# Optimization experiments

Measured on AMD Instinct MI355X. Metric: run time of the kernel, lower is better.

The kernel has to match this reference:

```python
import jax, jax.numpy as jnp
import numpy as np

DIM = 128
HEADS = 4
KV_RANK = 64
Q_RANK = 32
ROPE = DIM // 2   # 64
NOPE = DIM // 2   # 64
VDIM = DIM // 2   # 64
B, H, W = 2, 64, 64
EPS = 1e-5


def _conv1x1(x, w, b):
    # x: [B,C,H,W], w: [O,C], b: [O]
    return jnp.einsum('bchw,oc->bohw', x, w) + b[None, :, None, None]


def _gn1(x, g, b):
    # GroupNorm with 1 group: normalize over (C,H,W) per sample
    mu = jnp.mean(x, axis=(1, 2, 3), keepdims=True)
    var = jnp.mean((x - mu) ** 2, axis=(1, 2, 3), keepdims=True)
    return (x - mu) / jnp.sqrt(var + EPS) * g[None, :, None, None] + b[None, :, None, None]


def _freqs(h, w):
    # Replicates RotaryPositionalEncoding: pe[...,0::4]=sin_h, 1::4=cos_h, 2::4=sin_w, 3::4=cos_w
    n = ROPE // 4
    inv = 1.0 / (10000.0 ** (jnp.arange(n, dtype=jnp.float32) / n))
    ah = jnp.arange(h, dtype=jnp.float32)[:, None] * inv  # [h,n]
    aw = jnp.arange(w, dtype=jnp.float32)[:, None] * inv  # [w,n]
    fh = jnp.stack([jnp.sin(ah), jnp.cos(ah)], -1)  # [h,n,2] -> (real=sin_h, imag=cos_h)
    fw = jnp.stack([jnp.sin(aw), jnp.cos(aw)], -1)  # [w,n,2]
    fh_b = jnp.broadcast_to(fh[:, None], (h, w, n, 2))
    fw_b = jnp.broadcast_to(fw[None, :], (h, w, n, 2))
    # interleave pairs: pair 2m -> fh[m], pair 2m+1 -> fw[m]
    pe = jnp.stack([fh_b, fw_b], axis=3).reshape(h * w, ROPE // 2, 2)
    return pe  # [S, ROPE//2, 2]


def _rope(x, f):
    # x: [..., S, ROPE]; f: [S, ROPE//2, 2]
    xp = x.reshape(x.shape[:-1] + (ROPE // 2, 2))
    fr, fi = f[..., 0], f[..., 1]  # [S, ROPE//2] broadcast over leading dims
    rr = xp[..., 0] * fr - xp[..., 1] * fi
    ri = xp[..., 0] * fi + xp[..., 1] * fr
    return jnp.stack([rr, ri], -1).reshape(x.shape)


def setup_inputs() -> dict:
    key = jax.random.key(0)
    ks = jax.random.split(key, 8)
    s = 0.02
    inp = {
        'x': jax.random.normal(ks[0], (B, DIM, H, W), dtype=jnp.float32),
        'q1_w': jax.random.normal(ks[1], (Q_RANK, DIM), dtype=jnp.float32) * s,
        'q1_b': jnp.zeros((Q_RANK,), jnp.float32),
        'q_gn_g': jnp.ones((Q_RANK,), jnp.float32),
        'q_gn_b': jnp.zeros((Q_RANK,), jnp.float32),
        'q2_w': jax.random.normal(ks[2], (HEADS * (NOPE + ROPE), Q_RANK), dtype=jnp.float32) * s,
        'q2_b': jnp.zeros((HEADS * (NOPE + ROPE),), jnp.float32),
        'kv1_w': jax.random.normal(ks[3], (KV_RANK + ROPE, DIM), dtype=jnp.float32) * s,
        'kv1_b': jnp.zeros((KV_RANK + ROPE,), jnp.float32),
        'kv_gn_g': jnp.ones((KV_RANK + ROPE,), jnp.float32),
        'kv_gn_b': jnp.zeros((KV_RANK + ROPE,), jnp.float32),
        'kvn_g': jnp.ones((KV_RANK,), jnp.float32),
        'kvn_b': jnp.zeros((KV_RANK,), jnp.float32),
        'kvup_w': jax.random.normal(ks[4], (HEADS * (NOPE + VDIM), KV_RANK), dtype=jnp.float32) * s,
        'kvup_b': jnp.zeros((HEADS * (NOPE + VDIM),), jnp.float32),
        'out_w': jax.random.normal(ks[5], (DIM, HEADS * VDIM), dtype=jnp.float32) * s,
        'out_b': jnp.zeros((DIM,), jnp.float32),
    }
    return inp


def reference(x, q1_w, q1_b, q_gn_g, q_gn_b, q2_w, q2_b, kv1_w, kv1_b, kv_gn_g, kv_gn_b, kvn_g, kvn_b, kvup_w, kvup_b, out_w, out_b):
    b, c, h, w = x.shape
    s = h * w
    f = _freqs(h, w)  # [S, ROPE//2, 2]

    # Q path: low-rank down -> GN -> up
    q = _conv1x1(_gn1(_conv1x1(x, q1_w, q1_b), q_gn_g, q_gn_b), q2_w, q2_b)
    q = q.reshape(b, HEADS, NOPE + ROPE, s).transpose(0, 1, 3, 2)  # [B,H,S,D]
    q_nope, q_rope = q[..., :NOPE], q[..., NOPE:]
    q = jnp.concatenate([q_nope, _rope(q_rope, f)], axis=-1)

    # KV path: joint down-proj, split rope-k and compressed kv
    kv = _gn1(_conv1x1(x, kv1_w, kv1_b), kv_gn_g, kv_gn_b)  # [B, ROPE+KV_RANK, H, W]
    k_rope_c, kv_c = kv[:, :ROPE], kv[:, ROPE:]
    kv_u = _conv1x1(_gn1(kv_c, kvn_g, kvn_b), kvup_w, kvup_b)
    kv_u = kv_u.reshape(b, HEADS, NOPE + VDIM, s).transpose(0, 1, 3, 2)
    k_nope, v = kv_u[..., :NOPE], kv_u[..., NOPE:]

    k_rope = _rope(k_rope_c.reshape(b, ROPE, s).transpose(0, 2, 1)[:, None], f)  # [B,1,S,ROPE]
    k = jnp.concatenate([k_nope, jnp.broadcast_to(k_rope, (b, HEADS, s, ROPE))], axis=-1)

    scale = (NOPE + ROPE) ** -0.5
    attn = jax.nn.softmax(jnp.einsum('bhqd,bhkd->bhqk', q, k) * scale, axis=-1)
    o = jnp.einsum('bhqk,bhkd->bhqd', attn, v)  # [B,H,S,VDIM]
    o = o.transpose(0, 1, 3, 2).reshape(b, HEADS * VDIM, h, w)
    return _conv1x1(o, out_w, out_b) + x
```

## Files before the change

kernel.cpp:

```cpp
#include <hip/hip_runtime.h>

typedef unsigned short ushort_t;
typedef unsigned int uint_t;
typedef __attribute__((ext_vector_type(8))) short s16x8;
typedef __attribute__((ext_vector_type(4))) short s16x4;
typedef __attribute__((ext_vector_type(4))) float f32x4;
typedef __attribute__((ext_vector_type(16))) float f32x16;

#define S_TOT 4096
#define QSCALE 0.08838834764831845f
#define LOG2E 1.4426950408889634f
#define QSL (QSCALE * LOG2E)
#define L2_10000_D16 0.8304820237218406f

__device__ __forceinline__ ushort_t f2b(float f) {
  uint_t u = __float_as_uint(f);
  uint_t r = (u + 0x7FFFu + ((u >> 16) & 1u)) >> 16;
  return (ushort_t)r;
}

__device__ __forceinline__ float b2f(ushort_t u) {
  return __uint_as_float((uint_t)u << 16);
}

__device__ __forceinline__ uint_t cvt_pk_bf16(float lo, float hi) {
  uint_t r;
  asm("v_cvt_pk_bf16_f32 %0, %1, %2" : "=v"(r) : "v"(lo), "v"(hi));
  return r;
}

__device__ __forceinline__ void gload16(const void* g, void* l) {
  __builtin_amdgcn_global_load_lds(
      (const __attribute__((address_space(1))) unsigned int*)g,
      (__attribute__((address_space(3))) unsigned int*)l, 16, 0, 0);
}

__device__ __forceinline__ void rope_pair(float& x0, float& x1, int p, int hi, int wi, float scale) {
  float inv = exp2f(-(float)(p >> 1) * L2_10000_D16);
  float ang = ((p & 1) ? (float)wi : (float)hi) * inv;
  float sn = sinf(ang), cs = cosf(ang);
  float r0 = (x0 * sn - x1 * cs) * scale;
  float r1 = (x0 * cs + x1 * sn) * scale;
  x0 = r0; x1 = r1;
}

__global__ __launch_bounds__(256) void k_conv1(
    const float* __restrict__ x, const float* __restrict__ q1_w, const float* __restrict__ q1_b,
    const float* __restrict__ kv1_w, const float* __restrict__ kv1_b,
    float* __restrict__ y_q, float* __restrict__ y_kv, double* __restrict__ pch,
    const float* __restrict__ q2_w, const float* __restrict__ kvup_w,
    const float* __restrict__ out_w, ushort_t* __restrict__ wq2,
    ushort_t* __restrict__ wkvup, ushort_t* __restrict__ wout) {
  if (blockIdx.x >= 512) {
    int i = (blockIdx.x - 512) * 256 + threadIdx.x;
    if (i < 16384) wq2[i] = f2b(q2_w[i]);
    else if (i < 49152) wkvup[i - 16384] = f2b(kvup_w[i - 16384]);
    else if (i < 81920) wout[i - 49152] = f2b(out_w[i - 49152]);
    return;
  }
  const int b = blockIdx.x >> 8, blk = blockIdx.x & 255, st = blk * 16;
  const int t = threadIdx.x, si = t & 15, g = t >> 4;
  __shared__ float xs[128][16];
#pragma unroll
  for (int i = 0; i < 8; i++) {
    int c = g + 16 * i;
    xs[c][si] = x[(size_t)(b * 128 + c) * S_TOT + st + si];
  }
  __syncthreads();
  float acc[10];
#pragma unroll
  for (int i = 0; i < 10; i++) {
    int oc = g * 10 + i;
    acc[i] = (oc < 32) ? q1_b[oc] : kv1_b[oc - 32];
  }
  const float4* q1w4 = (const float4*)q1_w;
  const float4* kv1w4 = (const float4*)kv1_w;
  for (int c4 = 0; c4 < 32; c4++) {
    float x0 = xs[c4 * 4 + 0][si], x1 = xs[c4 * 4 + 1][si];
    float x2 = xs[c4 * 4 + 2][si], x3 = xs[c4 * 4 + 3][si];
#pragma unroll
    for (int i = 0; i < 10; i++) {
      int oc = g * 10 + i;
      float4 wv = (oc < 32) ? q1w4[oc * 32 + c4] : kv1w4[(oc - 32) * 32 + c4];
      acc[i] += wv.x * x0 + wv.y * x1 + wv.z * x2 + wv.w * x3;
    }
  }
#pragma unroll
  for (int i = 0; i < 10; i++) {
    int oc = g * 10 + i;
    float a = acc[i];
    if (oc < 32) y_q[(size_t)(b * 32 + oc) * S_TOT + st + si] = a;
    else         y_kv[(size_t)(b * 128 + oc - 32) * S_TOT + st + si] = a;
    double s = a, q = (double)a * a;
#pragma unroll
    for (int o = 1; o < 16; o <<= 1) { s += __shfl_xor(s, o, 16); q += __shfl_xor(q, o, 16); }
    if (si == 0) {
      double* pt = pch + (size_t)(b * 160 + oc) * 512 + blk * 2;
      pt[0] = s; pt[1] = q;
    }
  }
}

__global__ __launch_bounds__(256) void k_red(
    const double* __restrict__ pch, double* __restrict__ SQ) {
  const int pair = blockIdx.x, tid = threadIdx.x;
  const int lane = tid & 63, wid = tid >> 6;
  const double* p = pch + (size_t)pair * 512;
  double s = p[tid * 2], q = p[tid * 2 + 1];
#pragma unroll
  for (int o = 1; o < 64; o <<= 1) { s += __shfl_xor(s, o, 64); q += __shfl_xor(q, o, 64); }
  __shared__ double red[4][2];
  if (lane == 0) { red[wid][0] = s; red[wid][1] = q; }
  __syncthreads();
  if (tid == 0) {
    SQ[pair * 2]     = red[0][0] + red[1][0] + red[2][0] + red[3][0];
    SQ[pair * 2 + 1] = red[0][1] + red[1][1] + red[2][1] + red[3][1];
  }
}

__global__ __launch_bounds__(512) void k_stats(
    const double* __restrict__ SQ,
    const float* __restrict__ qg, const float* __restrict__ qb,
    const float* __restrict__ kvg, const float* __restrict__ kvb,
    const float* __restrict__ kng, const float* __restrict__ knb,
    float* __restrict__ coef) {
  __shared__ double Sh[2][160], Qh[2][160];
  const int tid = threadIdx.x;
  if (tid < 320) {
    int b = tid / 160, c = tid % 160;
    Sh[b][c] = SQ[tid * 2]; Qh[b][c] = SQ[tid * 2 + 1];
  }
  __syncthreads();
  if (tid < 2) {
    int b = tid;
    float* cf = coef + b * 320;
    const double NS = 4096.0;
    double muq = 0, m2q = 0;
    for (int c = 0; c < 32; c++) { muq += Sh[b][c]; m2q += Qh[b][c]; }
    muq /= (32.0 * NS); m2q /= (32.0 * NS);
    double rstdq = 1.0 / sqrt(m2q - muq * muq + 1e-5);
    for (int c = 0; c < 32; c++) {
      double A = rstdq * (double)qg[c];
      cf[c] = (float)A; cf[32 + c] = (float)((double)qb[c] - muq * A);
    }
    double mukv = 0, m2kv = 0;
    for (int c = 0; c < 128; c++) { mukv += Sh[b][32 + c]; m2kv += Qh[b][32 + c]; }
    mukv /= (128.0 * NS); m2kv /= (128.0 * NS);
    double rstdkv = 1.0 / sqrt(m2kv - mukv * mukv + 1e-5);
    for (int c = 0; c < 64; c++) {
      double A = rstdkv * (double)kvg[c];
      cf[64 + c] = (float)A; cf[128 + c] = (float)((double)kvb[c] - mukv * A);
    }
    double mu2 = 0, m22 = 0;
    for (int c2 = 0; c2 < 64; c2++) {
      int c = 64 + c2;
      double a = rstdkv * (double)kvg[c], bb = (double)kvb[c] - mukv * a;
      double Ec = Sh[b][32 + c] / NS, M2c = Qh[b][32 + c] / NS;
      mu2 += a * Ec + bb;
      m22 += a * a * M2c + 2.0 * a * bb * Ec + bb * bb;
    }
    mu2 /= 64.0; m22 /= 64.0;
    double rstd2 = 1.0 / sqrt(m22 - mu2 * mu2 + 1e-5);
    for (int c2 = 0; c2 < 64; c2++) {
      int c = 64 + c2;
      double a = rstdkv * (double)kvg[c], bb = (double)kvb[c] - mukv * a;
      cf[192 + c2] = (float)(a * rstd2 * (double)kng[c2]);
      cf[256 + c2] = (float)((bb - mu2) * rstd2 * (double)kng[c2] + (double)knb[c2]);
    }
  }
}

__global__ __launch_bounds__(256) void k_gq(
    const float* __restrict__ y_q, const float* __restrict__ coef,
    const ushort_t* __restrict__ wq2, const float* __restrict__ q2_b,
    ushort_t* __restrict__ Q) {
  const int id = blockIdx.x;
  const int h = id & 3, st = (id >> 2) & 63, b = id >> 8;
  const int t = threadIdx.x, si = t & 63, wid = t >> 6;
  const int l15 = t & 15, lg = (t >> 4) & 3;
  const float* cf = coef + b * 320;
  __shared__ __align__(16) ushort_t Xt[64][64];
  __shared__ __align__(16) ushort_t sQ[64][128];
  {
    ushort_t pk[8];
#pragma unroll
    for (int j = 0; j < 8; j++) {
      int c = wid * 8 + j;
      float v = y_q[(size_t)(b * 32 + c) * S_TOT + st * 64 + si];
      pk[j] = f2b(v * cf[c] + cf[32 + c]);
    }
    *(s16x8*)((char*)&Xt[si][0] + ((wid * 16) ^ ((si & 7) << 4))) = *(s16x8*)pk;
  }
  __syncthreads();
  const int d0w = wid * 32;
  f32x4 acc[2][4];
#pragma unroll
  for (int db = 0; db < 2; db++) {
    f32x4 bv;
#pragma unroll
    for (int r = 0; r < 4; r++) bv[r] = q2_b[h * 128 + d0w + db * 16 + lg * 4 + r];
#pragma unroll
    for (int sb = 0; sb < 4; sb++) acc[db][sb] = bv;
  }
  s16x8 wf[2];
#pragma unroll
  for (int db = 0; db < 2; db++)
    wf[db] = *(const s16x8*)(wq2 + (size_t)(h * 128 + d0w + db * 16 + l15) * 32 + lg * 8);
  const int xsw = (lg * 16) ^ ((l15 & 7) << 4);
#pragma unroll
  for (int sb = 0; sb < 4; sb++) {
    s16x8 xf = *(const s16x8*)((const char*)&Xt[sb * 16 + l15][0] + xsw);
#pragma unroll
    for (int db = 0; db < 2; db++)
      acc[db][sb] = __builtin_amdgcn_mfma_f32_16x16x32_bf16(wf[db], xf, acc[db][sb], 0, 0, 0);
  }
  if (wid >= 2) {
#pragma unroll
    for (int db = 0; db < 2; db++)
#pragma unroll
      for (int sb = 0; sb < 4; sb++) {
        int sp = st * 64 + sb * 16 + l15, hi = sp >> 6, wi = sp & 63;
        int dg = d0w + db * 16 + lg * 4;
#pragma unroll
        for (int pr = 0; pr < 2; pr++) {
          float v0 = acc[db][sb][pr * 2], v1 = acc[db][sb][pr * 2 + 1];
          int p = (dg + pr * 2 - 64) >> 1;
          rope_pair(v0, v1, p, hi, wi, QSL);
          acc[db][sb][pr * 2] = v0; acc[db][sb][pr * 2 + 1] = v1;
        }
      }
  } else {
#pragma unroll
    for (int db = 0; db < 2; db++)
#pragma unroll
      for (int sb = 0; sb < 4; sb++)
#pragma unroll
        for (int r = 0; r < 4; r++) acc[db][sb][r] *= QSL;
  }
#pragma unroll
  for (int db = 0; db < 2; db++)
#pragma unroll
    for (int sb = 0; sb < 4; sb++) {
      ushort_t pk[4];
#pragma unroll
      for (int r = 0; r < 4; r++) pk[r] = f2b(acc[db][sb][r]);
      int srow = sb * 16 + l15;
      *(s16x4*)((char*)&sQ[srow][0] + (((d0w + db * 16 + lg * 4) * 2) ^ ((srow & 7) << 4))) =
          *(s16x4*)pk;
    }
  __syncthreads();
  ushort_t* qrow = Q + ((size_t)(b * 4 + h) * S_TOT + st * 64 + si) * 128 + wid * 32;
#pragma unroll
  for (int j = 0; j < 4; j++) {
    s16x8 v = *(const s16x8*)((const char*)&sQ[si][0] + ((wid * 64 + j * 16) ^ ((si & 7) << 4)));
    *(s16x8*)(qrow + j * 8) = v;
  }
}

__global__ __launch_bounds__(256) void k_gkv(
    const float* __restrict__ y_kv, const float* __restrict__ coef,
    const ushort_t* __restrict__ wkvup, const float* __restrict__ kvup_b,
    ushort_t* __restrict__ K, ushort_t* __restrict__ VT) {
  const int id = blockIdx.x;
  const int h = id & 3, st = (id >> 2) & 63, b = id >> 8;
  const int t = threadIdx.x, si = t & 63, wid = t >> 6;
  const int l15 = t & 15, lg = (t >> 4) & 3;
  const float* cf = coef + b * 320;
  __shared__ __align__(16) ushort_t Xt[64][64];
  __shared__ __align__(16) ushort_t sK[64][64];
  {
#pragma unroll
    for (int half = 0; half < 2; half++) {
      ushort_t pk[8];
#pragma unroll
      for (int j = 0; j < 8; j++) {
        int c2 = wid * 16 + half * 8 + j;
        float v = y_kv[(size_t)(b * 128 + 64 + c2) * S_TOT + st * 64 + si];
        pk[j] = f2b(v * cf[192 + c2] + cf[256 + c2]);
      }
      *(s16x8*)((char*)&Xt[si][0] + ((wid * 32 + half * 16) ^ ((si & 7) << 4))) = *(s16x8*)pk;
    }
  }
  __syncthreads();
  const int d0w = wid * 32;
  f32x4 acc[2][4];
#pragma unroll
  for (int db = 0; db < 2; db++) {
    f32x4 bv;
#pragma unroll
    for (int r = 0; r < 4; r++) bv[r] = kvup_b[h * 128 + d0w + db * 16 + lg * 4 + r];
#pragma unroll
    for (int sb = 0; sb < 4; sb++) acc[db][sb] = bv;
  }
  s16x8 wf[2][2];
#pragma unroll
  for (int db = 0; db < 2; db++)
#pragma unroll
    for (int kk = 0; kk < 2; kk++)
      wf[db][kk] = *(const s16x8*)(wkvup + (size_t)(h * 128 + d0w + db * 16 + l15) * 64 +
                                   kk * 32 + lg * 8);
#pragma unroll
  for (int sb = 0; sb < 4; sb++) {
#pragma unroll
    for (int kk = 0; kk < 2; kk++) {
      s16x8 xf = *(const s16x8*)((const char*)&Xt[sb * 16 + l15][0] +
                                 ((kk * 64 + lg * 16) ^ ((l15 & 7) << 4)));
#pragma unroll
      for (int db = 0; db < 2; db++)
        acc[db][sb] = __builtin_amdgcn_mfma_f32_16x16x32_bf16(wf[db][kk], xf, acc[db][sb], 0, 0, 0);
    }
  }
  if (wid < 2) {
#pragma unroll
    for (int db = 0; db < 2; db++)
#pragma unroll
      for (int sb = 0; sb < 4; sb++) {
        ushort_t pk[4];
#pragma unroll
        for (int r = 0; r < 4; r++) pk[r] = f2b(acc[db][sb][r]);
        int srow = sb * 16 + l15;
        *(s16x4*)((char*)&sK[srow][0] + (((d0w + db * 16 + lg * 4) * 2) ^ ((srow & 7) << 4))) =
            *(s16x4*)pk;
      }
  } else {
    ushort_t* vb = VT + (size_t)(b * 4 + h) * 64 * S_TOT;
#pragma unroll
    for (int db = 0; db < 2; db++)
#pragma unroll
      for (int sb = 0; sb < 4; sb++) {
        int sp = st * 64 + sb * 16 + l15;
#pragma unroll
        for (int r = 0; r < 4; r++) {
          int vd = (wid - 2) * 32 + db * 16 + lg * 4 + r;
          vb[(size_t)vd * S_TOT + sp] = f2b(acc[db][sb][r]);
        }
      }
  }
  __syncthreads();
  const int sp = st * 64 + si;
  ushort_t* krow = K + ((size_t)(b * 4 + h) * S_TOT + sp) * 128;
#pragma unroll
  for (int j = 0; j < 2; j++) {
    s16x8 v = *(const s16x8*)((const char*)&sK[si][0] + ((wid * 32 + j * 16) ^ ((si & 7) << 4)));
    *(s16x8*)(krow + wid * 16 + j * 8) = v;
  }
  {
    const int c0 = wid * 16, hi = sp >> 6, wi = sp & 63;
    float v[16];
#pragma unroll
    for (int j = 0; j < 16; j++) {
      int c = c0 + j;
      v[j] = y_kv[(size_t)(b * 128 + c) * S_TOT + sp] * cf[64 + c] + cf[128 + c];
    }
#pragma unroll
    for (int k = 0; k < 8; k++) {
      int p = (c0 >> 1) + k;
      rope_pair(v[2 * k], v[2 * k + 1], p, hi, wi, 1.0f);
    }
    ushort_t pk[16];
#pragma unroll
    for (int j = 0; j < 16; j++) pk[j] = f2b(v[j]);
    *(s16x8*)(krow + 64 + c0) = *(s16x8*)pk;
    *(s16x8*)(krow + 64 + c0 + 8) = *(s16x8*)(pk + 8);
  }
}

__global__ __launch_bounds__(256, 2) void k_attn(
    const ushort_t* __restrict__ Q, const ushort_t* __restrict__ K,
    const ushort_t* __restrict__ VT, ushort_t* __restrict__ Opart,
    float* __restrict__ ml) {
  const int bid = blockIdx.x;
  const int bh = bid & 7;
  const int rest = bid >> 3;
  const int half = rest >> 5, qblk = rest & 31;
  const int kv0 = half * 2048;
  const int tid = threadIdx.x;
  const int wid = tid >> 6, lane = tid & 63;
  const int l31 = lane & 31, hi = lane >> 5;
  const int qbase = qblk * 128 + wid * 32;
  const ushort_t* Qp = Q + (size_t)bh * S_TOT * 128;
  const ushort_t* Kp = K + (size_t)bh * S_TOT * 128;
  const ushort_t* Vp = VT + (size_t)bh * 64 * S_TOT;

  __shared__ __align__(16) ushort_t K_lds[3][64][128];
  __shared__ __align__(16) ushort_t V_lds[3][64][64];

  s16x8 qf[8];
#pragma unroll
  for (int c = 0; c < 8; c++)
    qf[c] = *(const s16x8*)(Qp + (size_t)(qbase + l31) * 128 + c * 16 + hi * 8);

  f32x16 o0, o1;
#pragma unroll
  for (int r = 0; r < 16; r++) { o0[r] = 0.f; o1[r] = 0.f; }
  float m_s = -1e30f, l_s = 0.f;

  const int krow_l = tid >> 4;
  const int kcolb = (tid & 15) * 16;
  const int vrow_l = tid >> 3;
  const int vcolb = (tid & 7) * 16;

#define STAGE(kvb, bufi)                                                          \
  {                                                                               \
    _Pragma("unroll")                                                             \
    for (int i = 0; i < 4; i++) {                                                 \
      int row = i * 16 + krow_l;                                                  \
      int colb = kcolb ^ ((row & 15) << 4);                                       \
      gload16((const char*)(Kp + (size_t)((kvb) + row) * 128) + colb,             \
              (void*)&K_lds[bufi][i * 16 + wid * 4][0]);                          \
    }                                                                             \
    _Pragma("unroll")                                                             \
    for (int i = 0; i < 2; i++) {                                                 \
      int vd = i * 32 + vrow_l;                                                   \
      int colb = vcolb ^ ((vd & 7) << 4);                                         \
      gload16((const char*)(Vp + (size_t)vd * S_TOT + (kvb)) + colb,              \
              (void*)&V_lds[bufi][i * 32 + wid * 8][0]);                          \
    }                                                                             \
  }

  STAGE(kv0, 0);
  STAGE(kv0 + 64, 1);

  const int kswz = (l31 & 15) << 4;
  const int vswz = (l31 & 7) << 4;
#pragma unroll 1
  for (int t = 0; t < 32; t++) {
    const int buf = t % 3;
    if (t < 31) {
      asm volatile("s_waitcnt vmcnt(6)" ::: "memory");
    } else {
      asm volatile("s_waitcnt vmcnt(0)" ::: "memory");
    }
    __builtin_amdgcn_sched_barrier(0);
    __builtin_amdgcn_s_barrier();
    __builtin_amdgcn_sched_barrier(0);
    if (t < 30) STAGE(kv0 + (t + 2) * 64, (t + 2) % 3);
    f32x16 sc0, sc1;
#pragma unroll
    for (int r = 0; r < 16; r++) { sc0[r] = 0.f; sc1[r] = 0.f; }
    __builtin_amdgcn_s_setprio(1);
#pragma unroll
    for (int c = 0; c < 8; c++) {
      const int off = (c * 32 + hi * 16) ^ kswz;
      s16x8 k0 = *(const s16x8*)((const char*)&K_lds[buf][l31][0] + off);
      s16x8 k1 = *(const s16x8*)((const char*)&K_lds[buf][32 + l31][0] + off);
      sc0 = __builtin_amdgcn_mfma_f32_32x32x16_bf16(k0, qf[c], sc0, 0, 0, 0);
      sc1 = __builtin_amdgcn_mfma_f32_32x32x16_bf16(k1, qf[c], sc1, 0, 0, 0);
    }
    __builtin_amdgcn_s_setprio(0);
    float pmax;
    {
      float a = fmaxf(sc0[0], sc0[1]);
#pragma unroll
      for (int r = 2; r < 16; r++) a = fmaxf(a, sc0[r]);
#pragma unroll
      for (int r = 0; r < 16; r++) a = fmaxf(a, sc1[r]);
      pmax = a;
    }
    pmax = fmaxf(pmax, __shfl_xor(pmax, 32, 64));
    if (__any(pmax - m_s > 11.5f)) {
      float mn = fmaxf(m_s, pmax);
      float alpha = exp2f(m_s - mn);
      m_s = mn;
      l_s *= alpha;
#pragma unroll
      for (int r = 0; r < 16; r++) { o0[r] *= alpha; o1[r] *= alpha; }
    }
    float rs = 0.f;
#pragma unroll
    for (int r = 0; r < 16; r++) {
      float p0 = exp2f(sc0[r] - m_s);
      float p1 = exp2f(sc1[r] - m_s);
      sc0[r] = p0; sc1[r] = p1;
      rs += p0 + p1;
    }
    l_s += rs;
    __builtin_amdgcn_s_setprio(1);
#pragma unroll
    for (int c = 0; c < 4; c++) {
      const f32x16 P = (c < 2) ? sc0 : sc1;
      const int rA = 8 * (c & 1);
      uint_t a0 = cvt_pk_bf16(P[rA + 0], P[rA + 1]);
      uint_t a1 = cvt_pk_bf16(P[rA + 2], P[rA + 3]);
      uint_t b0 = cvt_pk_bf16(P[rA + 4], P[rA + 5]);
      uint_t b1 = cvt_pk_bf16(P[rA + 6], P[rA + 7]);
      uint_t s0 = hi ? a0 : b0, s1 = hi ? a1 : b1;
      uint_t r0 = (uint_t)__shfl_xor((int)s0, 32, 64);
      uint_t r1 = (uint_t)__shfl_xor((int)s1, 32, 64);
      union { uint_t u[4]; s16x8 v; } pf;
      pf.u[0] = hi ? r0 : a0; pf.u[1] = hi ? r1 : a1;
      pf.u[2] = hi ? b0 : r0; pf.u[3] = hi ? b1 : r1;
      const int voff = (c * 32 + hi * 16) ^ vswz;
      s16x8 v0 = *(const s16x8*)((const char*)&V_lds[buf][l31][0] + voff);
      s16x8 v1 = *(const s16x8*)((const char*)&V_lds[buf][32 + l31][0] + voff);
      o0 = __builtin_amdgcn_mfma_f32_32x32x16_bf16(v0, pf.v, o0, 0, 0, 0);
      o1 = __builtin_amdgcn_mfma_f32_32x32x16_bf16(v1, pf.v, o1, 0, 0, 0);
    }
    __builtin_amdgcn_s_setprio(0);
  }
#undef STAGE
  l_s += __shfl_xor(l_s, 32, 64);
  float linv = 1.f / l_s;
  if (lane < 32) {
    float* mlrow = ml + ((size_t)(half * 8 + bh) * S_TOT + qbase + l31) * 2;
    mlrow[0] = m_s; mlrow[1] = l_s;
  }
  char* sO = (char*)&K_lds[0][0][0];
#pragma unroll
  for (int vt = 0; vt < 2; vt++) {
#pragma unroll
    for (int r = 0; r < 16; r += 2) {
      float v0 = (vt ? o1[r] : o0[r]) * linv;
      float v1 = (vt ? o1[r + 1] : o0[r + 1]) * linv;
      uint_t u = cvt_pk_bf16(v0, v1);
      int vd = vt * 32 + (r & 3) + 8 * (r >> 2) + 4 * hi;
      *(uint_t*)(sO + (wid * 32 + l31) * 128 + ((vd * 2) ^ ((l31 & 7) << 4))) = u;
    }
  }
  __syncthreads();
  {
    const int r = tid >> 1, hf = tid & 1;
    const int w = r >> 5, ql = r & 31;
    ushort_t* orow = Opart + ((size_t)(half * 8 + bh) * S_TOT + qblk * 128 + r) * 64 + hf * 32;
#pragma unroll
    for (int j = 0; j < 4; j++) {
      s16x8 v = *(const s16x8*)(sO + (w * 32 + ql) * 128 + ((hf * 64 + j * 16) ^ ((ql & 7) << 4)));
      *(s16x8*)(orow + j * 8) = v;
    }
  }
}

__global__ __launch_bounds__(256) void k_oc(
    const ushort_t* __restrict__ Opart, const float* __restrict__ ml,
    const ushort_t* __restrict__ wout, const float* __restrict__ out_b,
    const float* __restrict__ x, float* __restrict__ out) {
  const int id = blockIdx.x;
  const int cch = id & 1, st32 = (id >> 1) & 127, b = id >> 8;
  const int t = threadIdx.x, wid = t >> 6;
  const int l15 = t & 15, lg = (t >> 4) & 3;
  __shared__ __align__(16) ushort_t Xt[32][256];
  {
    const int s = t & 31, grp = t >> 5;
    const int h = grp >> 1, vd0 = (grp & 1) * 32;
    const int sp = st32 * 32 + s;
    const float2 ml0 = *(const float2*)&ml[((size_t)(b * 4 + h) * S_TOT + sp) * 2];
    const float2 ml1 = *(const float2*)&ml[((size_t)(8 + b * 4 + h) * S_TOT + sp) * 2];
    float mm = fmaxf(ml0.x, ml1.x);
    float w0 = exp2f(ml0.x - mm) * ml0.y, w1 = exp2f(ml1.x - mm) * ml1.y;
    float inv = 1.f / (w0 + w1);
    w0 *= inv; w1 *= inv;
    const ushort_t* oa = Opart + ((size_t)(b * 4 + h) * S_TOT + sp) * 64 + vd0;
    const ushort_t* obp = oa + (size_t)8 * S_TOT * 64;
#pragma unroll
    for (int j4 = 0; j4 < 4; j4++) {
      union { s16x8 v; ushort_t u[8]; } av, bv2;
      av.v = *(const s16x8*)(oa + j4 * 8);
      bv2.v = *(const s16x8*)(obp + j4 * 8);
      ushort_t pk[8];
#pragma unroll
      for (int j = 0; j < 8; j++) pk[j] = f2b(w0 * b2f(av.u[j]) + w1 * b2f(bv2.u[j]));
      *(s16x8*)((char*)&Xt[s][0] + ((grp * 64 + j4 * 16) ^ ((s & 7) << 4))) = *(s16x8*)pk;
    }
  }
  __syncthreads();
  const int c0w = cch * 64 + wid * 16;
  f32x4 acc[2];
  {
    f32x4 bv;
#pragma unroll
    for (int r = 0; r < 4; r++) bv[r] = out_b[c0w + lg * 4 + r];
    acc[0] = bv; acc[1] = bv;
  }
#pragma unroll
  for (int kk = 0; kk < 8; kk++) {
    s16x8 wf = *(const s16x8*)(wout + (size_t)(c0w + l15) * 256 + kk * 32 + lg * 8);
#pragma unroll
    for (int sb = 0; sb < 2; sb++) {
      s16x8 xf = *(const s16x8*)((const char*)&Xt[sb * 16 + l15][0] +
                                 ((kk * 64 + lg * 16) ^ ((l15 & 7) << 4)));
      acc[sb] = __builtin_amdgcn_mfma_f32_16x16x32_bf16(wf, xf, acc[sb], 0, 0, 0);
    }
  }
#pragma unroll
  for (int sb = 0; sb < 2; sb++) {
#pragma unroll
    for (int r = 0; r < 4; r++) {
      int c = c0w + lg * 4 + r;
      int sp = st32 * 32 + sb * 16 + l15;
      size_t idx = (size_t)(b * 128 + c) * S_TOT + sp;
      out[idx] = acc[sb][r] + x[idx];
    }
  }
}

extern "C" void kernel_launch(void* const* d_in, const int* in_sizes, int n_in,
                              void* d_out, int out_size, void* d_ws, size_t ws_size,
                              hipStream_t stream) {
  const float* x      = (const float*)d_in[0];
  const float* q1_w   = (const float*)d_in[1];
  const float* q1_b   = (const float*)d_in[2];
  const float* q_gn_g = (const float*)d_in[3];
  const float* q_gn_b = (const float*)d_in[4];
  const float* q2_w   = (const float*)d_in[5];
  const float* q2_b   = (const float*)d_in[6];
  const float* kv1_w  = (const float*)d_in[7];
  const float* kv1_b  = (const float*)d_in[8];
  const float* kv_gn_g= (const float*)d_in[9];
  const float* kv_gn_b= (const float*)d_in[10];
  const float* kvn_g  = (const float*)d_in[11];
  const float* kvn_b  = (const float*)d_in[12];
  const float* kvup_w = (const float*)d_in[13];
  const float* kvup_b = (const float*)d_in[14];
  const float* out_w  = (const float*)d_in[15];
  const float* out_b  = (const float*)d_in[16];

  const size_t MB = 1u << 20;
  char* ws = (char*)d_ws;
  float*    y_q   = (float*)(ws);
  float*    y_kv  = (float*)(ws + 1 * MB);
  ushort_t* Q     = (ushort_t*)(ws + 5 * MB);
  ushort_t* K     = (ushort_t*)(ws + 13 * MB);
  ushort_t* VT    = (ushort_t*)(ws + 21 * MB);
  double*   pch   = (double*)(ws + 25 * MB);
  double*   SQ    = (double*)(ws + 26 * MB + 524288);
  float*    coef  = (float*)(ws + 26 * MB + 532480);
  ushort_t* wq2   = (ushort_t*)(ws + 26 * MB + 540672);
  ushort_t* wkvup = (ushort_t*)(ws + 26 * MB + 573440);
  ushort_t* wout  = (ushort_t*)(ws + 26 * MB + 638976);
  ushort_t* Opart = (ushort_t*)(ws + 27 * MB);
  float*    ml    = (float*)(ws + 36 * MB);
  float*    out   = (float*)d_out;

  k_conv1<<<832, 256, 0, stream>>>(x, q1_w, q1_b, kv1_w, kv1_b, y_q, y_kv, pch,
                                   q2_w, kvup_w, out_w, wq2, wkvup, wout);
  k_red  <<<320, 256, 0, stream>>>(pch, SQ);
  k_stats<<<1,   512, 0, stream>>>(SQ, q_gn_g, q_gn_b, kv_gn_g, kv_gn_b, kvn_g, kvn_b, coef);
  k_gq   <<<512, 256, 0, stream>>>(y_q, coef, wq2, q2_b, Q);
  k_gkv  <<<512, 256, 0, stream>>>(y_kv, coef, wkvup, kvup_b, K, VT);
  k_attn <<<512, 256, 0, stream>>>(Q, K, VT, Opart, ml);
  k_oc   <<<512, 256, 0, stream>>>(Opart, ml, wout, out_b, x, out);
}
```

Measured before the change: 152.4 us.

## Absorb kv up-projection into Q and output weights, share latent KV across heads

Folds the kv up-projection weights into the q2 projection (nope part) and the output projection, so attention operates directly on a shared per-batch latent KV instead of per-head K and V. The per-head K/V generation GEMM kernel is replaced by a light latent-normalization kernel, cutting K/V memory footprint and traffic by the head count. Weight folding is done on-device in the first kernel's spare blocks; the K-side bias is dropped as softmax-invariant and the V bias folded into the output bias. Risks slight numeric differences from bf16 rounding of folded weights and a low-parallelism latent kernel with strided writes.

```diff
diff --git a/kernel.cpp b/kernel.cpp
--- a/kernel.cpp
+++ b/kernel.cpp
@@ -48,14 +48,52 @@
     const float* __restrict__ x, const float* __restrict__ q1_w, const float* __restrict__ q1_b,
     const float* __restrict__ kv1_w, const float* __restrict__ kv1_b,
     float* __restrict__ y_q, float* __restrict__ y_kv, double* __restrict__ pch,
-    const float* __restrict__ q2_w, const float* __restrict__ kvup_w,
-    const float* __restrict__ out_w, ushort_t* __restrict__ wq2,
-    ushort_t* __restrict__ wkvup, ushort_t* __restrict__ wout) {
+    const float* __restrict__ q2_w, const float* __restrict__ q2_b,
+    const float* __restrict__ kvup_w, const float* __restrict__ kvup_b,
+    const float* __restrict__ out_w, const float* __restrict__ out_b,
+    ushort_t* __restrict__ wq2, ushort_t* __restrict__ wout,
+    float* __restrict__ q2b2, float* __restrict__ outb2) {
   if (blockIdx.x >= 512) {
-    int i = (blockIdx.x - 512) * 256 + threadIdx.x;
-    if (i < 16384) wq2[i] = f2b(q2_w[i]);
-    else if (i < 49152) wkvup[i - 16384] = f2b(kvup_w[i - 16384]);
-    else if (i < 81920) wout[i - 49152] = f2b(out_w[i - 49152]);
+    int E = (blockIdx.x - 512) * 256 + threadIdx.x;
+    if (E < 16384) {
+      int oc = E >> 5, r = E & 31;
+      int h = oc >> 7, d = oc & 127;
+      float val;
+      if (d < 64) {
+        val = 0.f;
+        for (int dd = 0; dd < 64; dd++)
+          val += kvup_w[(h * 128 + dd) * 64 + d] * q2_w[(size_t)(h * 128 + dd) * 32 + r];
+      } else {
+        val = q2_w[(size_t)oc * 32 + r];
+      }
+      wq2[(size_t)oc * 32 + r] = f2b(val);
+    } else if (E < 49152) {
+      int e = E - 16384;
+      int c = e >> 8, col = e & 255;
+      int h = col >> 6, l = col & 63;
+      float val = 0.f;
+      for (int vd = 0; vd < 64; vd++)
+        val += out_w[(size_t)c * 256 + h * 64 + vd] * kvup_w[(h * 128 + 64 + vd) * 64 + l];
+      wout[(size_t)c * 256 + col] = f2b(val);
+    } else if (E < 49664) {
+      int oc = E - 49152;
+      int h = oc >> 7, d = oc & 127;
+      float val;
+      if (d < 64) {
+        val = 0.f;
+        for (int dd = 0; dd < 64; dd++)
+          val += kvup_w[(h * 128 + dd) * 64 + d] * q2_b[h * 128 + dd];
+      } else val = q2_b[oc];
+      q2b2[oc] = val;
+    } else if (E < 49792) {
+      int c = E - 49664;
+      float val = out_b[c];
+      for (int j = 0; j < 256; j++) {
+        int h = j >> 6, vd = j & 63;
+        val += out_w[(size_t)c * 256 + j] * kvup_b[h * 128 + 64 + vd];
+      }
+      outb2[c] = val;
+    }
     return;
   }
   const int b = blockIdx.x >> 8, blk = blockIdx.x & 255, st = blk * 16;
@@ -172,7 +210,7 @@
 
 __global__ __launch_bounds__(256) void k_gq(
     const float* __restrict__ y_q, const float* __restrict__ coef,
-    const ushort_t* __restrict__ wq2, const float* __restrict__ q2_b,
+    const ushort_t* __restrict__ wq2, const float* __restrict__ q2b2,
     ushort_t* __restrict__ Q) {
   const int id = blockIdx.x;
   const int h = id & 3, st = (id >> 2) & 63, b = id >> 8;
@@ -198,7 +236,7 @@
   for (int db = 0; db < 2; db++) {
     f32x4 bv;
 #pragma unroll
-    for (int r = 0; r < 4; r++) bv[r] = q2_b[h * 128 + d0w + db * 16 + lg * 4 + r];
+    for (int r = 0; r < 4; r++) bv[r] = q2b2[h * 128 + d0w + db * 16 + lg * 4 + r];
 #pragma unroll
     for (int sb = 0; sb < 4; sb++) acc[db][sb] = bv;
   }
@@ -257,116 +295,51 @@
   }
 }
 
-__global__ __launch_bounds__(256) void k_gkv(
+__global__ __launch_bounds__(256) void k_lat(
     const float* __restrict__ y_kv, const float* __restrict__ coef,
-    const ushort_t* __restrict__ wkvup, const float* __restrict__ kvup_b,
-    ushort_t* __restrict__ K, ushort_t* __restrict__ VT) {
-  const int id = blockIdx.x;
-  const int h = id & 3, st = (id >> 2) & 63, b = id >> 8;
-  const int t = threadIdx.x, si = t & 63, wid = t >> 6;
-  const int l15 = t & 15, lg = (t >> 4) & 3;
+    ushort_t* __restrict__ C, ushort_t* __restrict__ VT) {
+  const int blk = blockIdx.x;
+  const int b = blk >> 6, st = (blk & 63) * 64;
+  const int t = threadIdx.x, si = t & 63, g = t >> 6;
   const float* cf = coef + b * 320;
-  __shared__ __align__(16) ushort_t Xt[64][64];
-  __shared__ __align__(16) ushort_t sK[64][64];
-  {
-#pragma unroll
-    for (int half = 0; half < 2; half++) {
-      ushort_t pk[8];
-#pragma unroll
-      for (int j = 0; j < 8; j++) {
-        int c2 = wid * 16 + half * 8 + j;
-        float v = y_kv[(size_t)(b * 128 + 64 + c2) * S_TOT + st * 64 + si];
-        pk[j] = f2b(v * cf[192 + c2] + cf[256 + c2]);
-      }
-      *(s16x8*)((char*)&Xt[si][0] + ((wid * 32 + half * 16) ^ ((si & 7) << 4))) = *(s16x8*)pk;
-    }
-  }
-  __syncthreads();
-  const int d0w = wid * 32;
-  f32x4 acc[2][4];
-#pragma unroll
-  for (int db = 0; db < 2; db++) {
-    f32x4 bv;
-#pragma unroll
-    for (int r = 0; r < 4; r++) bv[r] = kvup_b[h * 128 + d0w + db * 16 + lg * 4 + r];
-#pragma unroll
-    for (int sb = 0; sb < 4; sb++) acc[db][sb] = bv;
-  }
-  s16x8 wf[2][2];
-#pragma unroll
-  for (int db = 0; db < 2; db++)
-#pragma unroll
-    for (int kk = 0; kk < 2; kk++)
-      wf[db][kk] = *(const s16x8*)(wkvup + (size_t)(h * 128 + d0w + db * 16 + l15) * 64 +
-                                   kk * 32 + lg * 8);
-#pragma unroll
-  for (int sb = 0; sb < 4; sb++) {
-#pragma unroll
-    for (int kk = 0; kk < 2; kk++) {
-      s16x8 xf = *(const s16x8*)((const char*)&Xt[sb * 16 + l15][0] +
-                                 ((kk * 64 + lg * 16) ^ ((l15 & 7) << 4)));
-#pragma unroll
-      for (int db = 0; db < 2; db++)
-        acc[db][sb] = __builtin_amdgcn_mfma_f32_16x16x32_bf16(wf[db][kk], xf, acc[db][sb], 0, 0, 0);
-    }
-  }
-  if (wid < 2) {
-#pragma unroll
-    for (int db = 0; db < 2; db++)
-#pragma unroll
-      for (int sb = 0; sb < 4; sb++) {
-        ushort_t pk[4];
-#pragma unroll
-        for (int r = 0; r < 4; r++) pk[r] = f2b(acc[db][sb][r]);
-        int srow = sb * 16 + l15;
-        *(s16x4*)((char*)&sK[srow][0] + (((d0w + db * 16 + lg * 4) * 2) ^ ((srow & 7) << 4))) =
-            *(s16x4*)pk;
-      }
-  } else {
-    ushort_t* vb = VT + (size_t)(b * 4 + h) * 64 * S_TOT;
-#pragma unroll
-    for (int db = 0; db < 2; db++)
-#pragma unroll
-      for (int sb = 0; sb < 4; sb++) {
-        int sp = st * 64 + sb * 16 + l15;
-#pragma unroll
-        for (int r = 0; r < 4; r++) {
-          int vd = (wid - 2) * 32 + db * 16 + lg * 4 + r;
-          vb[(size_t)vd * S_TOT + sp] = f2b(acc[db][sb][r]);
-        }
-      }
-  }
-  __syncthreads();
-  const int sp = st * 64 + si;
-  ushort_t* krow = K + ((size_t)(b * 4 + h) * S_TOT + sp) * 128;
-#pragma unroll
-  for (int j = 0; j < 2; j++) {
-    s16x8 v = *(const s16x8*)((const char*)&sK[si][0] + ((wid * 32 + j * 16) ^ ((si & 7) << 4)));
-    *(s16x8*)(krow + wid * 16 + j * 8) = v;
-  }
-  {
-    const int c0 = wid * 16, hi = sp >> 6, wi = sp & 63;
-    float v[16];
-#pragma unroll
-    for (int j = 0; j < 16; j++) {
+  const int sp = st + si;
+  if (g < 2) {
+    const int c0 = g * 32;
+    float v[32];
+#pragma unroll
+    for (int j = 0; j < 32; j++) {
       int c = c0 + j;
       v[j] = y_kv[(size_t)(b * 128 + c) * S_TOT + sp] * cf[64 + c] + cf[128 + c];
     }
-#pragma unroll
-    for (int k = 0; k < 8; k++) {
-      int p = (c0 >> 1) + k;
-      rope_pair(v[2 * k], v[2 * k + 1], p, hi, wi, 1.0f);
-    }
-    ushort_t pk[16];
-#pragma unroll
-    for (int j = 0; j < 16; j++) pk[j] = f2b(v[j]);
-    *(s16x8*)(krow + 64 + c0) = *(s16x8*)pk;
-    *(s16x8*)(krow + 64 + c0 + 8) = *(s16x8*)(pk + 8);
+    const int hi = sp >> 6, wi = sp & 63;
+#pragma unroll
+    for (int k = 0; k < 16; k++)
+      rope_pair(v[2 * k], v[2 * k + 1], (c0 >> 1) + k, hi, wi, 1.0f);
+    ushort_t pk[32];
+#pragma unroll
+    for (int j = 0; j < 32; j++) pk[j] = f2b(v[j]);
+    ushort_t* crow = C + (size_t)(b * S_TOT + sp) * 128 + 64 + c0;
+#pragma unroll
+    for (int j4 = 0; j4 < 4; j4++) *(s16x8*)(crow + j4 * 8) = *(s16x8*)(pk + j4 * 8);
+  } else {
+    const int c0 = (g - 2) * 32;
+    ushort_t pk[32];
+#pragma unroll
+    for (int j = 0; j < 32; j++) {
+      int c2 = c0 + j;
+      float v = y_kv[(size_t)(b * 128 + 64 + c2) * S_TOT + sp] * cf[192 + c2] + cf[256 + c2];
+      ushort_t u = f2b(v);
+      pk[j] = u;
+      VT[(size_t)(b * 64 + c2) * S_TOT + sp] = u;
+    }
+    ushort_t* crow = C + (size_t)(b * S_TOT + sp) * 128 + c0;
+#pragma unroll
+    for (int j4 = 0; j4 < 4; j4++) *(s16x8*)(crow + j4 * 8) = *(s16x8*)(pk + j4 * 8);
   }
 }
 
 __global__ __launch_bounds__(256, 2) void k_attn(
-    const ushort_t* __restrict__ Q, const ushort_t* __restrict__ K,
+    const ushort_t* __restrict__ Q, const ushort_t* __restrict__ C,
     const ushort_t* __restrict__ VT, ushort_t* __restrict__ Opart,
     float* __restrict__ ml) {
   const int bid = blockIdx.x;
@@ -378,9 +351,10 @@
   const int wid = tid >> 6, lane = tid & 63;
   const int l31 = lane & 31, hi = lane >> 5;
   const int qbase = qblk * 128 + wid * 32;
+  const int b4 = bh >> 2;
   const ushort_t* Qp = Q + (size_t)bh * S_TOT * 128;
-  const ushort_t* Kp = K + (size_t)bh * S_TOT * 128;
-  const ushort_t* Vp = VT + (size_t)bh * 64 * S_TOT;
+  const ushort_t* Kp = C + (size_t)b4 * S_TOT * 128;
+  const ushort_t* Vp = VT + (size_t)b4 * 64 * S_TOT;
 
   __shared__ __align__(16) ushort_t K_lds[3][64][128];
   __shared__ __align__(16) ushort_t V_lds[3][64][64];
@@ -532,7 +506,7 @@
 
 __global__ __launch_bounds__(256) void k_oc(
     const ushort_t* __restrict__ Opart, const float* __restrict__ ml,
-    const ushort_t* __restrict__ wout, const float* __restrict__ out_b,
+    const ushort_t* __restrict__ wout, const float* __restrict__ outb2,
     const float* __restrict__ x, float* __restrict__ out) {
   const int id = blockIdx.x;
   const int cch = id & 1, st32 = (id >> 1) & 127, b = id >> 8;
@@ -568,7 +542,7 @@
   {
     f32x4 bv;
 #pragma unroll
-    for (int r = 0; r < 4; r++) bv[r] = out_b[c0w + lg * 4 + r];
+    for (int r = 0; r < 4; r++) bv[r] = outb2[c0w + lg * 4 + r];
     acc[0] = bv; acc[1] = bv;
   }
 #pragma unroll
@@ -619,24 +593,26 @@
   float*    y_q   = (float*)(ws);
   float*    y_kv  = (float*)(ws + 1 * MB);
   ushort_t* Q     = (ushort_t*)(ws + 5 * MB);
-  ushort_t* K     = (ushort_t*)(ws + 13 * MB);
-  ushort_t* VT    = (ushort_t*)(ws + 21 * MB);
-  double*   pch   = (double*)(ws + 25 * MB);
-  double*   SQ    = (double*)(ws + 26 * MB + 524288);
-  float*    coef  = (float*)(ws + 26 * MB + 532480);
-  ushort_t* wq2   = (ushort_t*)(ws + 26 * MB + 540672);
-  ushort_t* wkvup = (ushort_t*)(ws + 26 * MB + 573440);
-  ushort_t* wout  = (ushort_t*)(ws + 26 * MB + 638976);
-  ushort_t* Opart = (ushort_t*)(ws + 27 * MB);
-  float*    ml    = (float*)(ws + 36 * MB);
+  ushort_t* C     = (ushort_t*)(ws + 13 * MB);
+  ushort_t* VT    = (ushort_t*)(ws + 15 * MB);
+  double*   pch   = (double*)(ws + 17 * MB);
+  double*   SQ    = (double*)(ws + 19 * MB);
+  float*    coef  = (float*)(ws + 19 * MB + 8192);
+  ushort_t* wq2   = (ushort_t*)(ws + 19 * MB + 16384);
+  ushort_t* wout  = (ushort_t*)(ws + 19 * MB + 65536);
+  float*    q2b2  = (float*)(ws + 19 * MB + 131072);
+  float*    outb2 = (float*)(ws + 19 * MB + 139264);
+  ushort_t* Opart = (ushort_t*)(ws + 20 * MB);
+  float*    ml    = (float*)(ws + 28 * MB);
   float*    out   = (float*)d_out;
 
-  k_conv1<<<832, 256, 0, stream>>>(x, q1_w, q1_b, kv1_w, kv1_b, y_q, y_kv, pch,
-                                   q2_w, kvup_w, out_w, wq2, wkvup, wout);
+  k_conv1<<<707, 256, 0, stream>>>(x, q1_w, q1_b, kv1_w, kv1_b, y_q, y_kv, pch,
+                                   q2_w, q2_b, kvup_w, kvup_b, out_w, out_b,
+                                   wq2, wout, q2b2, outb2);
   k_red  <<<320, 256, 0, stream>>>(pch, SQ);
   k_stats<<<1,   512, 0, stream>>>(SQ, q_gn_g, q_gn_b, kv_gn_g, kv_gn_b, kvn_g, kvn_b, coef);
-  k_gq   <<<512, 256, 0, stream>>>(y_q, coef, wq2, q2_b, Q);
-  k_gkv  <<<512, 256, 0, stream>>>(y_kv, coef, wkvup, kvup_b, K, VT);
-  k_attn <<<512, 256, 0, stream>>>(Q, K, VT, Opart, ml);
-  k_oc   <<<512, 256, 0, stream>>>(Opart, ml, wout, out_b, x, out);
-}
+  k_gq   <<<512, 256, 0, stream>>>(y_q, coef, wq2, q2b2, Q);
+  k_lat  <<<128, 256, 0, stream>>>(y_kv, coef, C, VT);
+  k_attn <<<512, 256, 0, stream>>>(Q, C, VT, Opart, ml);
+  k_oc   <<<512, 256, 0, stream>>>(Opart, ml, wout, outb2, x, out);
+}
```

New measurement: 150.7 us. Within noise of the previous version (-1.1%).
